# Optimization experiments

Measured on AMD Instinct MI355X. Metric: run time of the kernel, lower is better.

The kernel has to match this reference:

```python
import jax, jax.numpy as jnp
import numpy as np

B, S, D = 8, 512, 1024
E, F, K = 8, 4096, 2


def setup_inputs() -> dict:
    key = jax.random.key(0)
    ks = jax.random.split(key, 8)
    scale = 1.0 / np.sqrt(D)
    return {
        "x": jax.random.normal(ks[0], (B, S, D), jnp.float32),
        "y": jax.random.randint(ks[1], (B,), 0, D),
        "W": jax.random.normal(ks[2], (D, D), jnp.float32) * scale,
        "b": jnp.zeros((D,), jnp.float32),
        "Wg": jax.random.normal(ks[3], (D, E), jnp.float32) * scale,
        "w1": jax.random.normal(ks[4], (E, D, F), jnp.float32) * scale,
        "b1": jnp.zeros((E, F), jnp.float32),
        "w2": jax.random.normal(ks[5], (E, F, D), jnp.float32) * (1.0 / np.sqrt(F)),
        "b2": jnp.zeros((E, D), jnp.float32),
    }


def reference(x, y, W, b, Wg, w1, b1, w2, b2):
    # linear projection (torch Linear convention: x @ W.T + b)
    lin = jnp.einsum("bsd,ed->bse", x, W) + b                      # [B,S,D]

    # --- MoE: top-2 softmax gate, renormalized over the top-k ---
    gate_logits = jnp.einsum("bsd,de->bse", lin, Wg)               # [B,S,E]
    probs = jax.nn.softmax(gate_logits, axis=-1)
    top_p, top_i = jax.lax.top_k(probs, K)                          # [B,S,K]
    top_p = top_p / jnp.sum(top_p, axis=-1, keepdims=True)
    # combine weights per expert: scatter top-k probs back to [B,S,E]
    gate = jnp.sum(jax.nn.one_hot(top_i, E, dtype=lin.dtype) * top_p[..., None], axis=-2)  # [B,S,E]

    # expert FFNs evaluated densely, combined by (sparse) gate weights
    h = jax.nn.relu(jnp.einsum("bsd,edf->ebsf", lin, w1) + b1[:, None, None, :])  # [E,B,S,F]
    expert_out = jnp.einsum("ebsf,efd->ebsd", h, w2) + b2[:, None, None, :]        # [E,B,S,D]
    moe_out = jnp.einsum("bse,ebsd->bsd", gate, expert_out)                        # [B,S,D]

    # residual, mean pool over sequence, cross-entropy
    sent_emb = jnp.mean(x + moe_out, axis=1)                       # [B,D] used as logits
    logp = jax.nn.log_softmax(sent_emb, axis=-1)
    loss = -jnp.mean(logp[jnp.arange(B), y])
    return loss
```

## Files before the change

kernel.cpp:

```cpp
#include <hip/hip_runtime.h>

#define TOK 4096
#define DD  1024
#define NE  8
#define FF  4096
#define NB  8
#define SS  512
#define HROWS 8320

typedef unsigned short ushort_t;
typedef __attribute__((ext_vector_type(8))) short bshort8;
typedef __attribute__((ext_vector_type(4))) float floatx4;

__device__ __forceinline__ ushort_t f2bf(float f) {
  unsigned int u = __float_as_uint(f);
  u += 0x7fffu + ((u >> 16) & 1u);
  return (ushort_t)(u >> 16);
}
__device__ __forceinline__ float bf2f(ushort_t h) {
  return __uint_as_float(((unsigned int)h) << 16);
}

__device__ __forceinline__ void gl_lds16(const ushort_t* g, ushort_t* l) {
  __builtin_amdgcn_global_load_lds(
      (const __attribute__((address_space(1))) unsigned int*)g,
      (__attribute__((address_space(3))) unsigned int*)l, 16, 0, 0);
}

__global__ __launch_bounds__(256) void k_cast(
    const float* __restrict__ in, ushort_t* __restrict__ out, int n4) {
  int i = blockIdx.x * 256 + threadIdx.x;
  if (i < n4) {
    float4 v = ((const float4*)in)[i];
    ushort4 o;
    o.x = f2bf(v.x); o.y = f2bf(v.y); o.z = f2bf(v.z); o.w = f2bf(v.w);
    ((ushort4*)out)[i] = o;
  }
}

__global__ __launch_bounds__(256) void k_transpose_cast(
    const float* __restrict__ in, size_t in_estride, int in_rstride,
    ushort_t* __restrict__ out, size_t out_estride, int out_rstride) {
  __shared__ ushort_t t[64][70];
  const float* ib = in + blockIdx.z * in_estride;
  ushort_t* ob = out + blockIdx.z * out_estride;
  const int r0 = blockIdx.y * 64, c0 = blockIdx.x * 64;
  const int tid = threadIdx.x;
  const int lr = tid >> 4, lc4 = (tid & 15) * 4;
#pragma unroll
  for (int it = 0; it < 4; ++it) {
    int r = lr + it * 16;
    float4 v = *(const float4*)&ib[(size_t)(r0 + r) * in_rstride + c0 + lc4];
    t[r][lc4 + 0] = f2bf(v.x);
    t[r][lc4 + 1] = f2bf(v.y);
    t[r][lc4 + 2] = f2bf(v.z);
    t[r][lc4 + 3] = f2bf(v.w);
  }
  __syncthreads();
  const int oc = tid >> 5, od2 = (tid & 31) * 2;
#pragma unroll
  for (int it = 0; it < 8; ++it) {
    int cc = oc + it * 8;
    ushort2 w;
    w.x = t[od2 + 0][cc];
    w.y = t[od2 + 1][cc];
    *(ushort2*)&ob[(size_t)(c0 + cc) * out_rstride + r0 + od2] = w;
  }
}

template <int MODE>
__global__ __launch_bounds__(256) void k_mfma(
    const ushort_t* __restrict__ A, const ushort_t* __restrict__ Bm,
    const float* __restrict__ bias, ushort_t* __restrict__ Obf,
    float* __restrict__ Of, const int* __restrict__ cnt,
    const int* __restrict__ offs, const int* __restrict__ btok, int f0,
    int accum, int kext, int ast, int ost, size_t bstride) {
  const int e = (MODE == 0) ? 0 : blockIdx.z;
  int c = TOK, off = 0;
  if (MODE != 0) {
    c = cnt[e];
    off = offs[e];
    if ((int)blockIdx.y * 128 >= c) return;
  }
  const int m0 = blockIdx.y * 128;
  const int n0 = blockIdx.x * 128;
  const ushort_t* Bp = (MODE == 0) ? Bm : Bm + (size_t)e * bstride;

  __shared__ ushort_t Als[128 * 32];
  __shared__ ushort_t Bls[128 * 32];
  __shared__ int ts[128];

  const int tid = threadIdx.x;
  if (tid < 128) {
    int p = m0 + tid;
    int r;
    if (MODE == 0) r = p;
    else if (MODE == 1) r = btok[e * TOK + min(p, c - 1)];
    else r = off + p;
    ts[tid] = r;
  }

  const int lane = tid & 63;
  const int w = tid >> 6;
  const int wm = (w & 1) * 64, wn = (w >> 1) * 64;
  const int lm = lane & 15, lq = lane >> 4;
  const int sr = lane >> 2;
  const int sg = lane & 3;

  floatx4 zero = {0.f, 0.f, 0.f, 0.f};
  floatx4 acc[4][4];
#pragma unroll
  for (int i = 0; i < 4; ++i)
#pragma unroll
    for (int j = 0; j < 4; ++j) acc[i][j] = zero;

  for (int k0 = 0; k0 < kext; k0 += 32) {
    __syncthreads();
#pragma unroll
    for (int i = 0; i < 2; ++i) {
      int r = w * 32 + i * 16 + sr;
      int q = (sg - (r >> 1)) & 3;
      const ushort_t* src = A + (size_t)ts[r] * ast + k0 + q * 8;
      ushort_t* dst = Als + r * 32 + sg * 8;
      gl_lds16(src, dst);
    }
#pragma unroll
    for (int i = 0; i < 2; ++i) {
      int r = w * 32 + i * 16 + sr;
      int q = (sg - (r >> 1)) & 3;
      const ushort_t* src = Bp + (size_t)(n0 + r) * kext + k0 + q * 8;
      ushort_t* dst = Bls + r * 32 + sg * 8;
      gl_lds16(src, dst);
    }
    __syncthreads();

    bshort8 af[4], bfr[4];
#pragma unroll
    for (int i = 0; i < 4; ++i) {
      int r = wm + i * 16 + lm;
      af[i] = *(const bshort8*)&Als[r * 32 + (((lq + (r >> 1)) & 3) * 8)];
    }
#pragma unroll
    for (int j = 0; j < 4; ++j) {
      int r = wn + j * 16 + lm;
      bfr[j] = *(const bshort8*)&Bls[r * 32 + (((lq + (r >> 1)) & 3) * 8)];
    }
#pragma unroll
    for (int i = 0; i < 4; ++i)
#pragma unroll
      for (int j = 0; j < 4; ++j)
        acc[i][j] = __builtin_amdgcn_mfma_f32_16x16x32_bf16(af[i], bfr[j],
                                                            acc[i][j], 0, 0, 0);
  }

#pragma unroll
  for (int i = 0; i < 4; ++i) {
#pragma unroll
    for (int j = 0; j < 4; ++j) {
      int n = wn + j * 16 + lm;
#pragma unroll
      for (int rr = 0; rr < 4; ++rr) {
        int m = wm + i * 16 + lq * 4 + rr;
        float v = acc[i][j][rr];
        if (MODE == 0) {
          int gn = n0 + n;
          v += bias[gn];
          Obf[(size_t)(m0 + m) * DD + gn] = f2bf(v);
        } else if (MODE == 1) {
          int p = m0 + m;
          if (p < c) {
            int gn = n0 + n;
            v += bias[(size_t)e * FF + f0 + gn];
            v = fmaxf(v, 0.f);
            Obf[(size_t)(off + p) * ost + gn] = f2bf(v);
          }
        } else {
          int p = m0 + m;
          if (p < c) {
            int gn = n0 + n;
            if (!accum) v += bias[(size_t)e * DD + gn];
            float* dp = &Of[(size_t)(off + p) * DD + gn];
            if (accum) *dp += v; else *dp = v;
          }
        }
      }
    }
  }
}

__global__ __launch_bounds__(256) void k_logits(
    const ushort_t* __restrict__ lin_bf, const float* __restrict__ Wg,
    int* __restrict__ topi, float* __restrict__ wts) {
  const int wv = threadIdx.x >> 6, lane = threadIdx.x & 63;
  const int t = blockIdx.x * 4 + wv;
  float acc[NE] = {};
  const ushort_t* lr = lin_bf + (size_t)t * DD;
#pragma unroll 4
  for (int d0 = 0; d0 < DD; d0 += 64) {
    float v = bf2f(lr[d0 + lane]);
    const float* wgr = Wg + (size_t)(d0 + lane) * NE;
    float4 g0 = *(const float4*)(wgr);
    float4 g1 = *(const float4*)(wgr + 4);
    acc[0] += v * g0.x; acc[1] += v * g0.y; acc[2] += v * g0.z; acc[3] += v * g0.w;
    acc[4] += v * g1.x; acc[5] += v * g1.y; acc[6] += v * g1.z; acc[7] += v * g1.w;
  }
#pragma unroll
  for (int off = 32; off > 0; off >>= 1) {
#pragma unroll
    for (int e = 0; e < NE; ++e) acc[e] += __shfl_xor(acc[e], off);
  }
  if (lane == 0) {
    int i1 = 0;
#pragma unroll
    for (int e = 1; e < NE; ++e)
      if (acc[e] > acc[i1]) i1 = e;
    int i2 = (i1 == 0) ? 1 : 0;
#pragma unroll
    for (int e = 0; e < NE; ++e)
      if (e != i1 && acc[e] > acc[i2]) i2 = e;
    float r = __expf(acc[i2] - acc[i1]);
    topi[t] = i1 | (i2 << 4);
    wts[2 * t + 0] = 1.0f / (1.0f + r);
    wts[2 * t + 1] = r / (1.0f + r);
  }
}

#define RT 512
__global__ __launch_bounds__(RT) void k_route(
    const int* __restrict__ topi, int* __restrict__ cnt, int* __restrict__ offs,
    int* __restrict__ btok, int* __restrict__ eslot) {
  __shared__ int sc[NE][RT + 1];
  __shared__ int tot[NE];
  const int tid = threadIdx.x;
  int lc[NE] = {};
  int my[8];
#pragma unroll
  for (int i = 0; i < 8; ++i) {
    int t = tid * 8 + i;
    int p = topi[t];
    my[i] = p;
    lc[p & 15]++;
    lc[(p >> 4) & 15]++;
  }
#pragma unroll
  for (int e = 0; e < NE; ++e) sc[e][tid] = lc[e];
  __syncthreads();
  if (tid < NE) {
    int s = 0;
    for (int i = 0; i < RT; ++i) { int v = sc[tid][i]; sc[tid][i] = s; s += v; }
    tot[tid] = s;
  }
  __syncthreads();
  if (tid == 0) {
    int s = 0;
    for (int e = 0; e < NE; ++e) { offs[e] = s; cnt[e] = tot[e]; s += tot[e]; }
  }
  __syncthreads();
  int run[NE];
#pragma unroll
  for (int e = 0; e < NE; ++e) run[e] = sc[e][tid];
#pragma unroll
  for (int i = 0; i < 8; ++i) {
    int t = tid * 8 + i, p = my[i];
    int e1 = p & 15, e2 = (p >> 4) & 15;
    int s1 = run[e1]++;
    btok[e1 * TOK + s1] = t;
    eslot[2 * t + 0] = e1 * TOK + s1;
    int s2 = run[e2]++;
    btok[e2 * TOK + s2] = t;
    eslot[2 * t + 1] = e2 * TOK + s2;
  }
}

__global__ __launch_bounds__(256) void k_pool(
    const float* __restrict__ x, const float* __restrict__ ob,
    const int* __restrict__ offs, const int* __restrict__ eslot,
    const float* __restrict__ wts, float* __restrict__ sent) {
  const int b = blockIdx.y;
  const int d = blockIdx.x * 256 + threadIdx.x;
  const int sc = blockIdx.z;
  float a = 0.f;
  for (int s = sc * 64; s < sc * 64 + 64; ++s) {
    int t = b * SS + s;
    int e0 = eslot[2 * t], e1 = eslot[2 * t + 1];
    int g0 = offs[e0 >> 12] + (e0 & (TOK - 1));
    int g1 = offs[e1 >> 12] + (e1 & (TOK - 1));
    a += x[(size_t)t * DD + d] + wts[2 * t] * ob[(size_t)g0 * DD + d] +
         wts[2 * t + 1] * ob[(size_t)g1 * DD + d];
  }
  atomicAdd(&sent[b * DD + d], a * (1.0f / SS));
}

__global__ __launch_bounds__(1024) void k_loss(
    const float* __restrict__ sent, const int* __restrict__ y,
    float* __restrict__ out) {
  __shared__ float red[16];
  const int tid = threadIdx.x;
  const int lane = tid & 63, wv = tid >> 6;
  float loss = 0.f;
  for (int b = 0; b < NB; ++b) {
    float v = sent[b * DD + tid];
    float m = v;
#pragma unroll
    for (int off = 32; off > 0; off >>= 1) m = fmaxf(m, __shfl_xor(m, off));
    if (lane == 0) red[wv] = m;
    __syncthreads();
    float m2 = red[0];
#pragma unroll
    for (int w = 1; w < 16; ++w) m2 = fmaxf(m2, red[w]);
    __syncthreads();
    float ex = __expf(v - m2);
#pragma unroll
    for (int off = 32; off > 0; off >>= 1) ex += __shfl_xor(ex, off);
    if (lane == 0) red[wv] = ex;
    __syncthreads();
    if (tid == 0) {
      float se = 0.f;
      for (int w = 0; w < 16; ++w) se += red[w];
      loss += m2 + logf(se) - sent[b * DD + y[b]];
    }
    __syncthreads();
  }
  if (tid == 0) out[0] = loss / NB;
}

extern "C" void kernel_launch(void* const* d_in, const int* in_sizes, int n_in,
                              void* d_out, int out_size, void* d_ws,
                              size_t ws_size, hipStream_t stream) {
  const float* x  = (const float*)d_in[0];
  const int*   y  = (const int*)d_in[1];
  const float* W  = (const float*)d_in[2];
  const float* bb = (const float*)d_in[3];
  const float* Wg = (const float*)d_in[4];
  const float* w1 = (const float*)d_in[5];
  const float* b1 = (const float*)d_in[6];
  const float* w2 = (const float*)d_in[7];
  const float* b2 = (const float*)d_in[8];
  float* out = (float*)d_out;

  auto need = [](size_t FCr) -> size_t {
    size_t o = 0;
    auto al = [&](size_t b) { o = (o + b + 255) & ~255ull; };
    al((size_t)TOK * DD * 2);
    al((size_t)TOK * DD * 2);
    al((size_t)DD * DD * 2);
    al((size_t)HROWS * FCr * 2);
    al((size_t)NE * FCr * DD * 2);
    al((size_t)NE * DD * FCr * 2);
    al((size_t)HROWS * DD * 4);
    al((size_t)NE * TOK * 4);
    al(64); al(64);
    al((size_t)TOK * 4);
    al((size_t)2 * TOK * 4);
    al((size_t)2 * TOK * 4);
    al((size_t)NB * DD * 4);
    return o;
  };
  const int nchunks = (ws_size >= need(FF)) ? 1 : 4;
  const int FCr = FF / nchunks;

  char* base = (char*)d_ws;
  size_t o = 0;
  auto al = [&](size_t b) -> char* {
    char* p = base + o;
    o = (o + b + 255) & ~255ull;
    return p;
  };
  ushort_t* lin_bf = (ushort_t*)al((size_t)TOK * DD * 2);
  ushort_t* x_bf   = (ushort_t*)al((size_t)TOK * DD * 2);
  ushort_t* W_bf   = (ushort_t*)al((size_t)DD * DD * 2);
  ushort_t* h_bf   = (ushort_t*)al((size_t)HROWS * FCr * 2);
  ushort_t* w1t    = (ushort_t*)al((size_t)NE * FCr * DD * 2);
  ushort_t* w2t    = (ushort_t*)al((size_t)NE * DD * FCr * 2);
  float*    ob     = (float*)al((size_t)HROWS * DD * 4);
  int*      btok   = (int*)al((size_t)NE * TOK * 4);
  int*      cnt    = (int*)al(64);
  int*      offs   = (int*)al(64);
  int*      topi   = (int*)al((size_t)TOK * 4);
  int*      eslot  = (int*)al((size_t)2 * TOK * 4);
  float*    wts    = (float*)al((size_t)2 * TOK * 4);
  float*    sent   = (float*)al((size_t)NB * DD * 4);

  hipMemsetAsync(sent, 0, NB * DD * sizeof(float), stream);

  k_cast<<<TOK * DD / 4 / 256, 256, 0, stream>>>(x, x_bf, TOK * DD / 4);
  k_cast<<<DD * DD / 4 / 256, 256, 0, stream>>>(W, W_bf, DD * DD / 4);

  k_mfma<0><<<dim3(DD / 128, TOK / 128), 256, 0, stream>>>(
      x_bf, W_bf, bb, lin_bf, nullptr, nullptr, nullptr, nullptr, 0, 0,
      DD, DD, DD, 0);

  k_logits<<<TOK / 4, 256, 0, stream>>>(lin_bf, Wg, topi, wts);
  k_route<<<1, RT, 0, stream>>>(topi, cnt, offs, btok, eslot);

  for (int ci = 0; ci < nchunks; ++ci) {
    int f0 = ci * FCr;
    k_transpose_cast<<<dim3(FCr / 64, DD / 64, NE), 256, 0, stream>>>(
        w1 + f0, (size_t)DD * FF, FF, w1t, (size_t)FCr * DD, DD);
    k_mfma<1><<<dim3(FCr / 128, TOK / 128, NE), 256, 0, stream>>>(
        lin_bf, w1t, b1, h_bf, nullptr, cnt, offs, btok, f0, 0,
        DD, DD, FCr, (size_t)FCr * DD);
    k_transpose_cast<<<dim3(DD / 64, FCr / 64, NE), 256, 0, stream>>>(
        w2 + (size_t)f0 * DD, (size_t)FF * DD, DD, w2t, (size_t)DD * FCr, FCr);
    k_mfma<2><<<dim3(DD / 128, TOK / 128, NE), 256, 0, stream>>>(
        h_bf, w2t, b2, nullptr, ob, cnt, offs, btok, f0, ci > 0 ? 1 : 0,
        FCr, FCr, DD, (size_t)DD * FCr);
  }

  k_pool<<<dim3(DD / 256, NB, 8), 256, 0, stream>>>(x, ob, offs, eslot, wts,
                                                    sent);
  k_loss<<<1, 1024, 0, stream>>>(sent, y, out);
}
```

Before: 688.3 us.

## Split-K second expert GEMM with atomics, widen K tile to 64, move b2 to pool

The down-projection expert GEMM is split along K into four slices. Each slice accumulates into a zeroed output buffer with float atomics, and the b2 bias is added later in the pooling kernel. The MFMA kernel's K tile grows from 32 to 64, with a new LDS swizzle, which halves the number of barrier pairs per tile. The weight transpose kernel now stages fp32 in LDS and writes 4-wide bf16 stores. The goal is more blocks for the down GEMM and less sync and store overhead, paid for with an extra memset of the output buffer and atomic contention.

```diff
diff --git a/kernel.cpp b/kernel.cpp
--- a/kernel.cpp
+++ b/kernel.cpp
@@ -41,7 +41,7 @@
 __global__ __launch_bounds__(256) void k_transpose_cast(
     const float* __restrict__ in, size_t in_estride, int in_rstride,
     ushort_t* __restrict__ out, size_t out_estride, int out_rstride) {
-  __shared__ ushort_t t[64][70];
+  __shared__ float t[64][65];
   const float* ib = in + blockIdx.z * in_estride;
   ushort_t* ob = out + blockIdx.z * out_estride;
   const int r0 = blockIdx.y * 64, c0 = blockIdx.x * 64;
@@ -51,20 +51,20 @@
   for (int it = 0; it < 4; ++it) {
     int r = lr + it * 16;
     float4 v = *(const float4*)&ib[(size_t)(r0 + r) * in_rstride + c0 + lc4];
-    t[r][lc4 + 0] = f2bf(v.x);
-    t[r][lc4 + 1] = f2bf(v.y);
-    t[r][lc4 + 2] = f2bf(v.z);
-    t[r][lc4 + 3] = f2bf(v.w);
+    t[r][lc4 + 0] = v.x; t[r][lc4 + 1] = v.y;
+    t[r][lc4 + 2] = v.z; t[r][lc4 + 3] = v.w;
   }
   __syncthreads();
-  const int oc = tid >> 5, od2 = (tid & 31) * 2;
-#pragma unroll
-  for (int it = 0; it < 8; ++it) {
-    int cc = oc + it * 8;
-    ushort2 w;
-    w.x = t[od2 + 0][cc];
-    w.y = t[od2 + 1][cc];
-    *(ushort2*)&ob[(size_t)(c0 + cc) * out_rstride + r0 + od2] = w;
+  const int od4 = (tid & 15) * 4, oc = tid >> 4;
+#pragma unroll
+  for (int it = 0; it < 4; ++it) {
+    int cc = oc + it * 16;
+    ushort4 w;
+    w.x = f2bf(t[od4 + 0][cc]);
+    w.y = f2bf(t[od4 + 1][cc]);
+    w.z = f2bf(t[od4 + 2][cc]);
+    w.w = f2bf(t[od4 + 3][cc]);
+    *(ushort4*)&ob[(size_t)(c0 + cc) * out_rstride + r0 + od4] = w;
   }
 }
 
@@ -74,8 +74,9 @@
     const float* __restrict__ bias, ushort_t* __restrict__ Obf,
     float* __restrict__ Of, const int* __restrict__ cnt,
     const int* __restrict__ offs, const int* __restrict__ btok, int f0,
-    int accum, int kext, int ast, int ost, size_t bstride) {
-  const int e = (MODE == 0) ? 0 : blockIdx.z;
+    int kext, int ast, int ost, size_t bstride, int nsplit, int klen) {
+  int e = 0, sp = 0;
+  if (MODE != 0) { e = blockIdx.z / nsplit; sp = blockIdx.z % nsplit; }
   int c = TOK, off = 0;
   if (MODE != 0) {
     c = cnt[e];
@@ -85,9 +86,10 @@
   const int m0 = blockIdx.y * 128;
   const int n0 = blockIdx.x * 128;
   const ushort_t* Bp = (MODE == 0) ? Bm : Bm + (size_t)e * bstride;
-
-  __shared__ ushort_t Als[128 * 32];
-  __shared__ ushort_t Bls[128 * 32];
+  const int kbeg = sp * klen, kfin = kbeg + klen;
+
+  __shared__ ushort_t Als[128 * 64];
+  __shared__ ushort_t Bls[128 * 64];
   __shared__ int ts[128];
 
   const int tid = threadIdx.x;
@@ -104,8 +106,8 @@
   const int w = tid >> 6;
   const int wm = (w & 1) * 64, wn = (w >> 1) * 64;
   const int lm = lane & 15, lq = lane >> 4;
-  const int sr = lane >> 2;
-  const int sg = lane & 3;
+  const int sr = lane >> 3;
+  const int sg = lane & 7;
 
   floatx4 zero = {0.f, 0.f, 0.f, 0.f};
   floatx4 acc[4][4];
@@ -114,43 +116,43 @@
 #pragma unroll
     for (int j = 0; j < 4; ++j) acc[i][j] = zero;
 
-  for (int k0 = 0; k0 < kext; k0 += 32) {
-    __syncthreads();
-#pragma unroll
-    for (int i = 0; i < 2; ++i) {
-      int r = w * 32 + i * 16 + sr;
-      int q = (sg - (r >> 1)) & 3;
-      const ushort_t* src = A + (size_t)ts[r] * ast + k0 + q * 8;
-      ushort_t* dst = Als + r * 32 + sg * 8;
-      gl_lds16(src, dst);
+  for (int k0 = kbeg; k0 < kfin; k0 += 64) {
+    __syncthreads();
+#pragma unroll
+    for (int i = 0; i < 4; ++i) {
+      int r = w * 32 + i * 8 + sr;
+      int q = (sg - r) & 7;
+      gl_lds16(A + (size_t)ts[r] * ast + k0 + q * 8, Als + r * 64 + sg * 8);
     }
 #pragma unroll
-    for (int i = 0; i < 2; ++i) {
-      int r = w * 32 + i * 16 + sr;
-      int q = (sg - (r >> 1)) & 3;
-      const ushort_t* src = Bp + (size_t)(n0 + r) * kext + k0 + q * 8;
-      ushort_t* dst = Bls + r * 32 + sg * 8;
-      gl_lds16(src, dst);
+    for (int i = 0; i < 4; ++i) {
+      int r = w * 32 + i * 8 + sr;
+      int q = (sg - r) & 7;
+      gl_lds16(Bp + (size_t)(n0 + r) * kext + k0 + q * 8,
+               Bls + r * 64 + sg * 8);
     }
     __syncthreads();
 
-    bshort8 af[4], bfr[4];
-#pragma unroll
-    for (int i = 0; i < 4; ++i) {
-      int r = wm + i * 16 + lm;
-      af[i] = *(const bshort8*)&Als[r * 32 + (((lq + (r >> 1)) & 3) * 8)];
+#pragma unroll
+    for (int kh = 0; kh < 2; ++kh) {
+      bshort8 af[4], bfr[4];
+#pragma unroll
+      for (int i = 0; i < 4; ++i) {
+        int r = wm + i * 16 + lm;
+        af[i] = *(const bshort8*)&Als[r * 64 + (((kh * 4 + lq + r) & 7) * 8)];
+      }
+#pragma unroll
+      for (int j = 0; j < 4; ++j) {
+        int r = wn + j * 16 + lm;
+        bfr[j] = *(const bshort8*)&Bls[r * 64 + (((kh * 4 + lq + r) & 7) * 8)];
+      }
+#pragma unroll
+      for (int i = 0; i < 4; ++i)
+#pragma unroll
+        for (int j = 0; j < 4; ++j)
+          acc[i][j] = __builtin_amdgcn_mfma_f32_16x16x32_bf16(
+              af[i], bfr[j], acc[i][j], 0, 0, 0);
     }
-#pragma unroll
-    for (int j = 0; j < 4; ++j) {
-      int r = wn + j * 16 + lm;
-      bfr[j] = *(const bshort8*)&Bls[r * 32 + (((lq + (r >> 1)) & 3) * 8)];
-    }
-#pragma unroll
-    for (int i = 0; i < 4; ++i)
-#pragma unroll
-      for (int j = 0; j < 4; ++j)
-        acc[i][j] = __builtin_amdgcn_mfma_f32_16x16x32_bf16(af[i], bfr[j],
-                                                            acc[i][j], 0, 0, 0);
   }
 
 #pragma unroll
@@ -177,10 +179,7 @@
         } else {
           int p = m0 + m;
           if (p < c) {
-            int gn = n0 + n;
-            if (!accum) v += bias[(size_t)e * DD + gn];
-            float* dp = &Of[(size_t)(off + p) * DD + gn];
-            if (accum) *dp += v; else *dp = v;
+            atomicAdd(&Of[(size_t)(off + p) * DD + n0 + n], v);
           }
         }
       }
@@ -274,8 +273,9 @@
 
 __global__ __launch_bounds__(256) void k_pool(
     const float* __restrict__ x, const float* __restrict__ ob,
-    const int* __restrict__ offs, const int* __restrict__ eslot,
-    const float* __restrict__ wts, float* __restrict__ sent) {
+    const float* __restrict__ b2, const int* __restrict__ offs,
+    const int* __restrict__ eslot, const float* __restrict__ wts,
+    float* __restrict__ sent) {
   const int b = blockIdx.y;
   const int d = blockIdx.x * 256 + threadIdx.x;
   const int sc = blockIdx.z;
@@ -283,10 +283,12 @@
   for (int s = sc * 64; s < sc * 64 + 64; ++s) {
     int t = b * SS + s;
     int e0 = eslot[2 * t], e1 = eslot[2 * t + 1];
-    int g0 = offs[e0 >> 12] + (e0 & (TOK - 1));
-    int g1 = offs[e1 >> 12] + (e1 & (TOK - 1));
-    a += x[(size_t)t * DD + d] + wts[2 * t] * ob[(size_t)g0 * DD + d] +
-         wts[2 * t + 1] * ob[(size_t)g1 * DD + d];
+    int x0 = e0 >> 12, x1 = e1 >> 12;
+    int g0 = offs[x0] + (e0 & (TOK - 1));
+    int g1 = offs[x1] + (e1 & (TOK - 1));
+    a += x[(size_t)t * DD + d] +
+         wts[2 * t + 0] * (ob[(size_t)g0 * DD + d] + b2[x0 * DD + d]) +
+         wts[2 * t + 1] * (ob[(size_t)g1 * DD + d] + b2[x1 * DD + d]);
   }
   atomicAdd(&sent[b * DD + d], a * (1.0f / SS));
 }
@@ -358,6 +360,7 @@
   };
   const int nchunks = (ws_size >= need(FF)) ? 1 : 4;
   const int FCr = FF / nchunks;
+  const int nsplit = (nchunks == 1) ? 4 : 1;
 
   char* base = (char*)d_ws;
   size_t o = 0;
@@ -382,13 +385,14 @@
   float*    sent   = (float*)al((size_t)NB * DD * 4);
 
   hipMemsetAsync(sent, 0, NB * DD * sizeof(float), stream);
+  hipMemsetAsync(ob, 0, (size_t)HROWS * DD * 4, stream);
 
   k_cast<<<TOK * DD / 4 / 256, 256, 0, stream>>>(x, x_bf, TOK * DD / 4);
   k_cast<<<DD * DD / 4 / 256, 256, 0, stream>>>(W, W_bf, DD * DD / 4);
 
   k_mfma<0><<<dim3(DD / 128, TOK / 128), 256, 0, stream>>>(
-      x_bf, W_bf, bb, lin_bf, nullptr, nullptr, nullptr, nullptr, 0, 0,
-      DD, DD, DD, 0);
+      x_bf, W_bf, bb, lin_bf, nullptr, nullptr, nullptr, nullptr, 0,
+      DD, DD, DD, 0, 1, DD);
 
   k_logits<<<TOK / 4, 256, 0, stream>>>(lin_bf, Wg, topi, wts);
   k_route<<<1, RT, 0, stream>>>(topi, cnt, offs, btok, eslot);
@@ -398,16 +402,16 @@
     k_transpose_cast<<<dim3(FCr / 64, DD / 64, NE), 256, 0, stream>>>(
         w1 + f0, (size_t)DD * FF, FF, w1t, (size_t)FCr * DD, DD);
     k_mfma<1><<<dim3(FCr / 128, TOK / 128, NE), 256, 0, stream>>>(
-        lin_bf, w1t, b1, h_bf, nullptr, cnt, offs, btok, f0, 0,
-        DD, DD, FCr, (size_t)FCr * DD);
+        lin_bf, w1t, b1, h_bf, nullptr, cnt, offs, btok, f0,
+        DD, DD, FCr, (size_t)FCr * DD, 1, DD);
     k_transpose_cast<<<dim3(DD / 64, FCr / 64, NE), 256, 0, stream>>>(
         w2 + (size_t)f0 * DD, (size_t)FF * DD, DD, w2t, (size_t)DD * FCr, FCr);
-    k_mfma<2><<<dim3(DD / 128, TOK / 128, NE), 256, 0, stream>>>(
-        h_bf, w2t, b2, nullptr, ob, cnt, offs, btok, f0, ci > 0 ? 1 : 0,
-        FCr, FCr, DD, (size_t)DD * FCr);
-  }
-
-  k_pool<<<dim3(DD / 256, NB, 8), 256, 0, stream>>>(x, ob, offs, eslot, wts,
-                                                    sent);
+    k_mfma<2><<<dim3(DD / 128, TOK / 128, NE * nsplit), 256, 0, stream>>>(
+        h_bf, w2t, nullptr, nullptr, ob, cnt, offs, btok, f0,
+        FCr, FCr, DD, (size_t)DD * FCr, nsplit, FCr / nsplit);
+  }
+
+  k_pool<<<dim3(DD / 256, NB, 8), 256, 0, stream>>>(x, ob, b2, offs, eslot,
+                                                    wts, sent);
   k_loss<<<1, 1024, 0, stream>>>(sent, y, out);
 }
```

New measurement: 708.1 us. 2.9% more time.
